# Kernel tuning notes

Measured on AMD Instinct MI355X. Metric: run time of the kernel, lower is better.

Reference implementation:

```python
import jax, jax.numpy as jnp
import numpy as np
from jax import lax

CHUNK = 64
GATING_C = 8.0
B, L, H, D = 4, 4096, 16, 128


def setup_inputs() -> dict:
    key = jax.random.key(0)
    ks = jax.random.split(key, 7)
    return {
        "alpha": jax.random.uniform(ks[0], (B, L, H), jnp.float32),
        "omega": jax.random.normal(ks[1], (B, L, H), jnp.float32),
        "dt": jax.random.uniform(ks[2], (B, L, H), jnp.float32),
        "K": jax.random.normal(ks[3], (B, L, H, D), jnp.float32),
        "V": jax.random.normal(ks[4], (B, L, H, 2), jnp.float32),
        "beta": jax.random.uniform(ks[5], (B, L, H), jnp.float32),
        "r_gate": jax.random.uniform(ks[6], (B, L, H), jnp.float32),
    }


def _build_A_bar(alpha, omega, dt, r_gate):
    # Cayley (bilinear) discretization of 2x2 Hamiltonian dynamics.
    tau = dt * 0.5
    ta = tau * alpha
    to = tau * omega
    denom = (1.0 + ta) ** 2 + to ** 2 + 1e-6
    inv_det = 1.0 / denom
    a11 = ((1.0 + ta) * (1.0 - ta) - to ** 2) * inv_det
    a12 = 2.0 * to * inv_det
    A_bar = jnp.stack([jnp.stack([a11, a12], axis=-1),
                       jnp.stack([-a12, a11], axis=-1)], axis=-2)  # (B,L,H,2,2)
    # recurrence-gate eigenvalue modulation
    numer = (1.0 - ta) ** 2 + to ** 2
    denom_e = (1.0 + ta) ** 2 + to ** 2
    eig_sq = numer / (denom_e + 1e-6)
    exponent = (GATING_C * r_gate - 1.0) * 0.5
    scale = jnp.clip(eig_sq, 1e-8, None) ** exponent
    return A_bar * scale[..., None, None]


def _intra_chunk_scan(A_f, K_f, V_f, beta_f, dt_f):
    # A_f:(BN,C,H,2,2) K_f:(BN,C,H,D) V_f:(BN,C,H,2) beta_f,dt_f:(BN,C,H)
    BN, C, Hh, Dd = K_f.shape
    h0 = jnp.zeros((BN, Hh, 2, Dd), jnp.float32)
    A0 = jnp.broadcast_to(jnp.eye(2, dtype=jnp.float32), (BN, Hh, 2, 2))

    def step(carry, xs):
        h, curr_A = carry
        A_t, k_t, v_t, b_t, dt_t = xs
        kTh = jnp.einsum('bhsd,bhd->bhs', h, k_t)             # retrieval (BN,H,2)
        b_e = b_t[..., None, None]
        h_mod = h - b_e * (kTh[..., None] * k_t[:, :, None, :])  # selective erasure
        h_new = (jnp.einsum('bhij,bhjd->bhid', A_t, h_mod)
                 + b_e * (v_t[..., None] * k_t[:, :, None, :]) * dt_t[..., None, None])
        curr_A = jnp.einsum('bhij,bhjk->bhik', A_t, curr_A)
        return (h_new, curr_A), (h_new, curr_A)

    xs = (jnp.swapaxes(A_f, 0, 1), jnp.swapaxes(K_f, 0, 1), jnp.swapaxes(V_f, 0, 1),
          jnp.swapaxes(beta_f, 0, 1), jnp.swapaxes(dt_f, 0, 1))
    _, (local_h, cum_A) = lax.scan(step, (h0, A0), xs)
    # time-first -> (BN,C,...)
    return jnp.swapaxes(local_h, 0, 1), jnp.swapaxes(cum_A, 0, 1)


def _inter_chunk_scan(total_A, final_h):
    # total_A:(B,NC,H,2,2) final_h:(B,NC,H,2,D)
    Bb, NC, Hh, _, Dd = final_h.shape
    s0 = jnp.zeros((Bb, Hh, 2, Dd), jnp.float32)

    def step(state, xs):
        tA, fh = xs
        new = jnp.einsum('bhij,bhjd->bhid', tA, state) + fh
        return new, state  # emit pre-update state (state entering chunk k)

    _, states = lax.scan(step, s0, (jnp.swapaxes(total_A, 0, 1), jnp.swapaxes(final_h, 0, 1)))
    return jnp.swapaxes(states, 0, 1)  # (B,NC,H,2,D)


def reference(alpha, omega, dt, K, V, beta, r_gate):
    Bb, Ll, Hh, Dd = K.shape
    C = CHUNK
    n_chunks = Ll // C  # L chosen divisible by chunk size (pad_len = 0)
    A_bar = _build_A_bar(alpha, omega, dt, r_gate)  # (B,L,H,2,2)

    A_f = A_bar.reshape(Bb * n_chunks, C, Hh, 2, 2)
    K_f = K.reshape(Bb * n_chunks, C, Hh, Dd)
    V_f = V.reshape(Bb * n_chunks, C, Hh, 2)
    beta_f = beta.reshape(Bb * n_chunks, C, Hh)
    dt_f = dt.reshape(Bb * n_chunks, C, Hh)

    local_h, cum_A = _intra_chunk_scan(A_f, K_f, V_f, beta_f, dt_f)
    local_h = local_h.reshape(Bb, n_chunks, C, Hh, 2, Dd)
    cum_A = cum_A.reshape(Bb, n_chunks, C, Hh, 2, 2)

    chunk_states = _inter_chunk_scan(cum_A[:, :, -1], local_h[:, :, -1])
    correction = jnp.einsum('bnchij,bnhjd->bnchid', cum_A, chunk_states)
    Y = (local_h + correction).reshape(Bb, Ll, Hh, 2, Dd)
    return Y, chunk_states
```

## Files before the change

kernel.cpp:

```cpp
#include <hip/hip_runtime.h>


namespace {

constexpr int NB  = 4;
constexpr int NL  = 4096;
constexpr int NH  = 16;
constexpr int ND  = 128;
constexpr int CHK = 64;
constexpr int NCH = NL / CHK;
constexpr int NTUP = NB * NCH * NH;
constexpr long long Y_FLOATS  = (long long)NB * NL * NH * 2 * ND;
constexpr int FH_FLOATS = NB * NCH * NH * 2 * ND;

template<bool WRITE_Y>
__global__ __launch_bounds__(256, 4)
void intra_scan(const float* __restrict__ alpha, const float* __restrict__ omega,
                const float* __restrict__ dtp,   const float* __restrict__ K,
                const float* __restrict__ V,     const float* __restrict__ beta,
                const float* __restrict__ rg,
                float* __restrict__ final_h, float* __restrict__ total_A,
                const float* __restrict__ chunk_states, float* __restrict__ Y)
{
    const int wid  = (int)((blockIdx.x * blockDim.x + threadIdx.x) >> 6);
    const int lane = threadIdx.x & 63;
    if (wid >= NTUP) return;
    const int h = wid & (NH - 1);
    const int n = (wid >> 4) & (NCH - 1);
    const int b = wid >> 10;

    const int gi0 = (b * NL + n * CHK) * NH + h;
    const float2* __restrict__ K2 = (const float2*)K;
    const float2* __restrict__ V2 = (const float2*)V;

    float h0x = 0.f, h0y = 0.f, h1x = 0.f, h1y = 0.f;
    float C00 = 1.f, C01 = 0.f, C10 = 0.f, C11 = 1.f;

    float S0x = 0.f, S0y = 0.f, S1x = 0.f, S1y = 0.f;
    if constexpr (WRITE_Y) {
        const float2* __restrict__ S2 = (const float2*)chunk_states;
        const int sb = ((b * NCH + n) * NH + h) * 128;
        const float2 s0 = S2[sb + lane];
        const float2 s1 = S2[sb + 64 + lane];
        S0x = s0.x; S0y = s0.y; S1x = s1.x; S1y = s1.y;
    }

    #pragma unroll 4
    for (int t = 0; t < CHK; ++t) {
        const int gi = gi0 + t * NH;
        const float a   = alpha[gi];
        const float w   = omega[gi];
        const float dtv = dtp[gi];
        const float be  = beta[gi];
        const float r   = rg[gi];
        const float2 vv = V2[gi];
        const float2 kk = K2[((size_t)gi << 6) + lane];

        const float tau  = 0.5f * dtv;
        const float ta   = tau * a;
        const float to   = tau * w;
        const float opta = 1.f + ta, omta = 1.f - ta;
        const float to2  = to * to;
        const float den  = opta * opta + to2 + 1e-6f;
        const float inv  = 1.f / den;
        const float a11  = (opta * omta - to2) * inv;
        const float a12  = (2.f * to) * inv;
        const float numer = omta * omta + to2;
        const float eig   = numer * inv;
        const float ex    = 4.f * r - 0.5f;
        const float sc    = exp2f(ex * log2f(fmaxf(eig, 1e-8f)));
        const float A00 = a11 * sc, A01 = a12 * sc;
        const float A10 = -(a12 * sc), A11v = a11 * sc;

        float p0 = h0x * kk.x + h0y * kk.y;
        float p1 = h1x * kk.x + h1y * kk.y;
        #pragma unroll
        for (int m = 1; m < 64; m <<= 1) {
            p0 += __shfl_xor(p0, m, 64);
            p1 += __shfl_xor(p1, m, 64);
        }

        const float bk0 = be * p0, bk1 = be * p1;
        const float hm0x = h0x - bk0 * kk.x, hm0y = h0y - bk0 * kk.y;
        const float hm1x = h1x - bk1 * kk.x, hm1y = h1y - bk1 * kk.y;
        const float bdt = be * dtv;
        const float sv0 = bdt * vv.x, sv1 = bdt * vv.y;
        h0x = A00 * hm0x + A01 * hm1x + sv0 * kk.x;
        h0y = A00 * hm0y + A01 * hm1y + sv0 * kk.y;
        h1x = A10 * hm0x + A11v * hm1x + sv1 * kk.x;
        h1y = A10 * hm0y + A11v * hm1y + sv1 * kk.y;

        const float c00 = A00 * C00 + A01 * C10;
        const float c01 = A00 * C01 + A01 * C11;
        const float c10 = A10 * C00 + A11v * C10;
        const float c11 = A10 * C01 + A11v * C11;
        C00 = c00; C01 = c01; C10 = c10; C11 = c11;

        if constexpr (WRITE_Y) {
            float2* __restrict__ Y2 = (float2*)Y;
            const int yb = gi << 7;
            float2 y0, y1;
            y0.x = h0x + c00 * S0x + c01 * S1x;
            y0.y = h0y + c00 * S0y + c01 * S1y;
            y1.x = h1x + c10 * S0x + c11 * S1x;
            y1.y = h1y + c10 * S0y + c11 * S1y;
            Y2[yb + lane]      = y0;
            Y2[yb + 64 + lane] = y1;
        }
    }

    if constexpr (!WRITE_Y) {
        float2* __restrict__ FH2 = (float2*)final_h;
        const int fb = wid * 128;
        FH2[fb + lane]      = make_float2(h0x, h0y);
        FH2[fb + 64 + lane] = make_float2(h1x, h1y);
        if (lane == 0) {
            ((float4*)total_A)[wid] = make_float4(C00, C01, C10, C11);
        }
    }
}

__global__ __launch_bounds__(128)
void inter_scan(const float* __restrict__ final_h, const float* __restrict__ total_A,
                float* __restrict__ states_out)
{
    const int bh = blockIdx.x;
    const int b = bh >> 4, h = bh & 15;
    const int d = threadIdx.x;
    float s0 = 0.f, s1 = 0.f;
    #pragma unroll 8
    for (int nn = 0; nn < NCH; ++nn) {
        const int tup  = (b * NCH + nn) * NH + h;
        const int base = tup * 256 + d;
        states_out[base]       = s0;
        states_out[base + 128] = s1;
        const float4 A  = ((const float4*)total_A)[tup];
        const float f0  = final_h[base];
        const float f1  = final_h[base + 128];
        const float ns0 = A.x * s0 + A.y * s1 + f0;
        const float ns1 = A.z * s0 + A.w * s1 + f1;
        s0 = ns0; s1 = ns1;
    }
}

}

extern "C" void kernel_launch(void* const* d_in, const int* in_sizes, int n_in,
                              void* d_out, int out_size, void* d_ws, size_t ws_size,
                              hipStream_t stream)
{
    const float* alpha = (const float*)d_in[0];
    const float* omega = (const float*)d_in[1];
    const float* dtp   = (const float*)d_in[2];
    const float* K     = (const float*)d_in[3];
    const float* V     = (const float*)d_in[4];
    const float* beta  = (const float*)d_in[5];
    const float* rg    = (const float*)d_in[6];

    float* Y       = (float*)d_out;
    float* states  = Y + Y_FLOATS;
    float* final_h = (float*)d_ws;
    float* total_A = final_h + FH_FLOATS;

    const dim3 blk(256);
    const dim3 grid(NTUP / 4);

    intra_scan<false><<<grid, blk, 0, stream>>>(alpha, omega, dtp, K, V, beta, rg,
                                                final_h, total_A, nullptr, nullptr);
    inter_scan<<<dim3(NB * NH), dim3(128), 0, stream>>>(final_h, total_A, states);
    intra_scan<true><<<grid, blk, 0, stream>>>(alpha, omega, dtp, K, V, beta, rg,
                                               nullptr, nullptr, states, Y);
}
```

Measured before the change: 465.7 us.

## Precompute per-step gates lane-parallel, use DPP reductions and prefetch K rows

The intra-chunk scan now has each lane compute the Cayley gate coefficients for one timestep up front, then broadcasts them with readlane inside the sequential loop instead of recomputing them redundantly in every lane. The wave-wide dot-product reduction uses DPP row ops plus a swizzle in place of six shfl_xor steps. The update algebra is refolded to exploit the skew-symmetric A so fewer multiplies sit on the dependency chain. K rows are software-prefetched in groups of four, and the inter-chunk scan stages total_A in LDS and keeps an 8-deep register ring of final_h loads. It relies on CHK equaling the wave size, and the early-return guard is removed.

Measured after the change: 443.9 us. 1.05x faster.

```diff
diff --git a/kernel.cpp b/kernel.cpp
--- a/kernel.cpp
+++ b/kernel.cpp
@@ -6,12 +6,31 @@
 constexpr int NB  = 4;
 constexpr int NL  = 4096;
 constexpr int NH  = 16;
-constexpr int ND  = 128;
 constexpr int CHK = 64;
 constexpr int NCH = NL / CHK;
 constexpr int NTUP = NB * NCH * NH;
-constexpr long long Y_FLOATS  = (long long)NB * NL * NH * 2 * ND;
-constexpr int FH_FLOATS = NB * NCH * NH * 2 * ND;
+constexpr long long Y_FLOATS  = (long long)NB * NL * NH * 2 * 128;
+constexpr int FH_FLOATS = NB * NCH * NH * 2 * 128;
+
+__device__ __forceinline__ float rl(float x, int l) {
+    return __int_as_float(__builtin_amdgcn_readlane(__float_as_int(x), l));
+}
+
+template<int CTRL>
+__device__ __forceinline__ float dpp_add(float x) {
+    int y = __builtin_amdgcn_update_dpp(0, __float_as_int(x), CTRL, 0xF, 0xF, false);
+    return x + __int_as_float(y);
+}
+
+__device__ __forceinline__ float wave_allsum(float x) {
+    x = dpp_add<0x121>(x);
+    x = dpp_add<0x122>(x);
+    x = dpp_add<0x124>(x);
+    x = dpp_add<0x128>(x);
+    x += __int_as_float(__builtin_amdgcn_ds_swizzle(__float_as_int(x), 0x401F));
+    x += __shfl_xor(x, 32, 64);
+    return x;
+}
 
 template<bool WRITE_Y>
 __global__ __launch_bounds__(256, 4)
@@ -24,7 +43,6 @@
 {
     const int wid  = (int)((blockIdx.x * blockDim.x + threadIdx.x) >> 6);
     const int lane = threadIdx.x & 63;
-    if (wid >= NTUP) return;
     const int h = wid & (NH - 1);
     const int n = (wid >> 4) & (NCH - 1);
     const int b = wid >> 10;
@@ -33,8 +51,35 @@
     const float2* __restrict__ K2 = (const float2*)K;
     const float2* __restrict__ V2 = (const float2*)V;
 
-    float h0x = 0.f, h0y = 0.f, h1x = 0.f, h1y = 0.f;
-    float C00 = 1.f, C01 = 0.f, C10 = 0.f, C11 = 1.f;
+    {
+    }
+    const int gl = gi0 + lane * NH;
+    const float a   = alpha[gl];
+    const float w   = omega[gl];
+    const float dtv = dtp[gl];
+    const float be  = beta[gl];
+    const float r   = rg[gl];
+    const float2 vv = V2[gl];
+
+    const float tau  = 0.5f * dtv;
+    const float ta   = tau * a;
+    const float to   = tau * w;
+    const float opta = 1.f + ta, omta = 1.f - ta;
+    const float to2  = to * to;
+    const float den  = opta * opta + to2 + 1e-6f;
+    const float inv  = 1.f / den;
+    const float a11  = (opta * omta - to2) * inv;
+    const float a12  = (2.f * to) * inv;
+    const float eig  = (omta * omta + to2) * inv;
+    const float ex   = 4.f * r - 0.5f;
+    const float sc   = exp2f(ex * log2f(fmaxf(eig, 1e-8f)));
+    const float A00L = a11 * sc;
+    const float A01L = a12 * sc;
+    const float eb0L = be * A00L;
+    const float eb1L = be * A01L;
+    const float bdt  = be * dtv;
+    const float sv0L = bdt * vv.x;
+    const float sv1L = bdt * vv.y;
 
     float S0x = 0.f, S0y = 0.f, S1x = 0.f, S1y = 0.f;
     if constexpr (WRITE_Y) {
@@ -45,68 +90,68 @@
         S0x = s0.x; S0y = s0.y; S1x = s1.x; S1y = s1.y;
     }
 
-    #pragma unroll 4
-    for (int t = 0; t < CHK; ++t) {
-        const int gi = gi0 + t * NH;
-        const float a   = alpha[gi];
-        const float w   = omega[gi];
-        const float dtv = dtp[gi];
-        const float be  = beta[gi];
-        const float r   = rg[gi];
-        const float2 vv = V2[gi];
-        const float2 kk = K2[((size_t)gi << 6) + lane];
-
-        const float tau  = 0.5f * dtv;
-        const float ta   = tau * a;
-        const float to   = tau * w;
-        const float opta = 1.f + ta, omta = 1.f - ta;
-        const float to2  = to * to;
-        const float den  = opta * opta + to2 + 1e-6f;
-        const float inv  = 1.f / den;
-        const float a11  = (opta * omta - to2) * inv;
-        const float a12  = (2.f * to) * inv;
-        const float numer = omta * omta + to2;
-        const float eig   = numer * inv;
-        const float ex    = 4.f * r - 0.5f;
-        const float sc    = exp2f(ex * log2f(fmaxf(eig, 1e-8f)));
-        const float A00 = a11 * sc, A01 = a12 * sc;
-        const float A10 = -(a12 * sc), A11v = a11 * sc;
-
-        float p0 = h0x * kk.x + h0y * kk.y;
-        float p1 = h1x * kk.x + h1y * kk.y;
+    const float2* __restrict__ kp = K2 + (((size_t)gi0) << 6) + lane;
+    float2* __restrict__ yp = nullptr;
+    if constexpr (WRITE_Y) yp = ((float2*)Y) + (((size_t)gi0) << 7) + lane;
+
+    float h0x = 0.f, h0y = 0.f, h1x = 0.f, h1y = 0.f;
+    float C00 = 1.f, C01 = 0.f, C10 = 0.f, C11 = 1.f;
+
+    float2 cur[4], nxt[4];
+    #pragma unroll
+    for (int j = 0; j < 4; ++j) cur[j] = kp[j * 1024];
+
+    for (int g = 0; g < 16; ++g) {
+        if (g < 15) {
+            #pragma unroll
+            for (int j = 0; j < 4; ++j) nxt[j] = kp[(g * 4 + 4 + j) * 1024];
+        }
         #pragma unroll
-        for (int m = 1; m < 64; m <<= 1) {
-            p0 += __shfl_xor(p0, m, 64);
-            p1 += __shfl_xor(p1, m, 64);
-        }
-
-        const float bk0 = be * p0, bk1 = be * p1;
-        const float hm0x = h0x - bk0 * kk.x, hm0y = h0y - bk0 * kk.y;
-        const float hm1x = h1x - bk1 * kk.x, hm1y = h1y - bk1 * kk.y;
-        const float bdt = be * dtv;
-        const float sv0 = bdt * vv.x, sv1 = bdt * vv.y;
-        h0x = A00 * hm0x + A01 * hm1x + sv0 * kk.x;
-        h0y = A00 * hm0y + A01 * hm1y + sv0 * kk.y;
-        h1x = A10 * hm0x + A11v * hm1x + sv1 * kk.x;
-        h1y = A10 * hm0y + A11v * hm1y + sv1 * kk.y;
-
-        const float c00 = A00 * C00 + A01 * C10;
-        const float c01 = A00 * C01 + A01 * C11;
-        const float c10 = A10 * C00 + A11v * C10;
-        const float c11 = A10 * C01 + A11v * C11;
-        C00 = c00; C01 = c01; C10 = c10; C11 = c11;
-
-        if constexpr (WRITE_Y) {
-            float2* __restrict__ Y2 = (float2*)Y;
-            const int yb = gi << 7;
-            float2 y0, y1;
-            y0.x = h0x + c00 * S0x + c01 * S1x;
-            y0.y = h0y + c00 * S0y + c01 * S1y;
-            y1.x = h1x + c10 * S0x + c11 * S1x;
-            y1.y = h1y + c10 * S0y + c11 * S1y;
-            Y2[yb + lane]      = y0;
-            Y2[yb + 64 + lane] = y1;
-        }
+        for (int j = 0; j < 4; ++j) {
+            const int t = g * 4 + j;
+            const float2 kk = cur[j];
+
+            const float A00 = rl(A00L, t);
+            const float A01 = rl(A01L, t);
+            const float eb0 = rl(eb0L, t);
+            const float eb1 = rl(eb1L, t);
+            const float sv0 = rl(sv0L, t);
+            const float sv1 = rl(sv1L, t);
+
+            float p0 = h0x * kk.x + h0y * kk.y;
+            float p1 = h1x * kk.x + h1y * kk.y;
+            p0 = wave_allsum(p0);
+            p1 = wave_allsum(p1);
+
+            const float R0x = A00 * h0x + A01 * h1x;
+            const float R0y = A00 * h0y + A01 * h1y;
+            const float R1x = A00 * h1x - A01 * h0x;
+            const float R1y = A00 * h1y - A01 * h0y;
+
+            const float c0 = sv0 - (eb0 * p0 + eb1 * p1);
+            const float c1 = sv1 - (eb0 * p1 - eb1 * p0);
+
+            h0x = R0x + c0 * kk.x;  h0y = R0y + c0 * kk.y;
+            h1x = R1x + c1 * kk.x;  h1y = R1y + c1 * kk.y;
+
+            const float nc00 = A00 * C00 + A01 * C10;
+            const float nc01 = A00 * C01 + A01 * C11;
+            const float nc10 = A00 * C10 - A01 * C00;
+            const float nc11 = A00 * C11 - A01 * C01;
+            C00 = nc00; C01 = nc01; C10 = nc10; C11 = nc11;
+
+            if constexpr (WRITE_Y) {
+                float2 y0, y1;
+                y0.x = h0x + C00 * S0x + C01 * S1x;
+                y0.y = h0y + C00 * S0y + C01 * S1y;
+                y1.x = h1x + C10 * S0x + C11 * S1x;
+                y1.y = h1y + C10 * S0y + C11 * S1y;
+                yp[t * 2048]      = y0;
+                yp[t * 2048 + 64] = y1;
+            }
+        }
+        #pragma unroll
+        for (int j = 0; j < 4; ++j) cur[j] = nxt[j];
     }
 
     if constexpr (!WRITE_Y) {
@@ -127,19 +172,35 @@
     const int bh = blockIdx.x;
     const int b = bh >> 4, h = bh & 15;
     const int d = threadIdx.x;
+
+    __shared__ float4 As[NCH];
+    if (d < NCH) As[d] = ((const float4*)total_A)[(b * NCH + d) * NH + h];
+    __syncthreads();
+
+    float fa[8], fb[8];
+    #pragma unroll
+    for (int j = 0; j < 8; ++j) {
+        const int base = ((b * NCH + j) * NH + h) * 256 + d;
+        fa[j] = final_h[base];
+        fb[j] = final_h[base + 128];
+    }
+
     float s0 = 0.f, s1 = 0.f;
     #pragma unroll 8
     for (int nn = 0; nn < NCH; ++nn) {
-        const int tup  = (b * NCH + nn) * NH + h;
-        const int base = tup * 256 + d;
+        const int slot = nn & 7;
+        const int base = ((b * NCH + nn) * NH + h) * 256 + d;
         states_out[base]       = s0;
         states_out[base + 128] = s1;
-        const float4 A  = ((const float4*)total_A)[tup];
-        const float f0  = final_h[base];
-        const float f1  = final_h[base + 128];
-        const float ns0 = A.x * s0 + A.y * s1 + f0;
-        const float ns1 = A.z * s0 + A.w * s1 + f1;
-        s0 = ns0; s1 = ns1;
+        const float4 A = As[nn];
+        const float n0 = A.x * s0 + A.y * s1 + fa[slot];
+        const float n1 = A.z * s0 + A.w * s1 + fb[slot];
+        s0 = n0; s1 = n1;
+        if (nn < NCH - 8) {
+            const int nb = ((b * NCH + nn + 8) * NH + h) * 256 + d;
+            fa[slot] = final_h[nb];
+            fb[slot] = final_h[nb + 128];
+        }
     }
 }
 
```
